# Kernel tuning notes

Hardware: AMD Instinct MI355X
Metric: run time of the kernel (lower is better)

## Reference

```python
import jax, jax.numpy as jnp
import numpy as np

N_FOOD = 50000
N_NUT = 50000
E = 800000
D = 128      # embedding_dim == hidden_dim
H = 4        # heads
C = D // H   # per-head channels
L = 2        # num_layers
NEG_SLOPE = 0.2


def _gat_conv(x_src, x_dst, ei, Wsrc, Wdst, a_src, a_dst, bias, n_dst):
    """PyG GATConv (bipartite, no self loops, concat heads, no edge_dim)."""
    hs = (x_src @ Wsrc).reshape(-1, H, C)   # [Ns, H, C]
    hd = (x_dst @ Wdst).reshape(-1, H, C)   # [Nd, H, C]
    src, dst = ei[0], ei[1]
    alpha_s = jnp.einsum('nhc,hc->nh', hs, a_src)  # [Ns, H]
    alpha_d = jnp.einsum('nhc,hc->nh', hd, a_dst)  # [Nd, H]
    e = alpha_s[src] + alpha_d[dst]                # [E, H]
    e = jax.nn.leaky_relu(e, NEG_SLOPE)
    # segment softmax over edges grouped by destination node
    emax = jax.ops.segment_max(e, dst, num_segments=n_dst)
    emax = jnp.where(jnp.isfinite(emax), emax, 0.0)
    ex = jnp.exp(e - emax[dst])
    denom = jax.ops.segment_sum(ex, dst, num_segments=n_dst)
    alpha = ex / (denom[dst] + 1e-16)              # [E, H]
    msg = hs[src] * alpha[:, :, None]              # [E, H, C]
    out = jax.ops.segment_sum(msg, dst, num_segments=n_dst)
    return out.reshape(n_dst, H * C) + bias


def setup_inputs() -> dict:
    key = jax.random.key(0)
    ks = jax.random.split(key, 16)
    w = 1.0 / np.sqrt(D)
    a = 1.0 / np.sqrt(C)
    inp = {
        'x_food': jax.random.normal(ks[0], (N_FOOD, D), jnp.float32),
        'x_nut': jax.random.normal(ks[1], (N_NUT, D), jnp.float32),
        'Wsrc_fn': jax.random.normal(ks[2], (L, D, D), jnp.float32) * w,
        'Wdst_fn': jax.random.normal(ks[3], (L, D, D), jnp.float32) * w,
        'att_src_fn': jax.random.normal(ks[4], (L, H, C), jnp.float32) * a,
        'att_dst_fn': jax.random.normal(ks[5], (L, H, C), jnp.float32) * a,
        'bias_fn': jnp.zeros((L, D), jnp.float32),
        'Wsrc_nf': jax.random.normal(ks[6], (L, D, D), jnp.float32) * w,
        'Wdst_nf': jax.random.normal(ks[7], (L, D, D), jnp.float32) * w,
        'att_src_nf': jax.random.normal(ks[8], (L, H, C), jnp.float32) * a,
        'att_dst_nf': jax.random.normal(ks[9], (L, H, C), jnp.float32) * a,
        'bias_nf': jnp.zeros((L, D), jnp.float32),
        'ei_fn': jax.random.randint(ks[10], (2, E), 0, N_FOOD, jnp.int32),  # food -> nutrient
        'ei_nf': jax.random.randint(ks[11], (2, E), 0, N_NUT, jnp.int32),   # nutrient -> food
    }
    return inp


def reference(x_food, x_nut, Wsrc_fn, Wdst_fn, att_src_fn, att_dst_fn, bias_fn,
              Wsrc_nf, Wdst_nf, att_src_nf, att_dst_nf, bias_nf, ei_fn, ei_nf):
    h_food, h_nut = x_food, x_nut
    for l in range(L):
        # relation food --contains--> nutrient (dst = nutrient)
        out_nut = _gat_conv(h_food, h_nut, ei_fn, Wsrc_fn[l], Wdst_fn[l],
                            att_src_fn[l], att_dst_fn[l], bias_fn[l], N_NUT)
        # relation nutrient --contained_in--> food (dst = food)
        out_food = _gat_conv(h_nut, h_food, ei_nf, Wsrc_nf[l], Wdst_nf[l],
                             att_src_nf[l], att_dst_nf[l], bias_nf[l], N_FOOD)
        # dropout is identity at inference; ELU activation
        h_food = jax.nn.elu(out_food)
        h_nut = jax.nn.elu(out_nut)
    return jnp.stack([h_food, h_nut])  # [2, 50000, 128]
```

## Files before the change

kernel.cpp:

```cpp
#include <hip/hip_runtime.h>
#include <math.h>

#define NNODE 50000
#define NEDGE 800000
#define DIM   128
#define NHEAD 4
#define NTILE ((NNODE + 63) / 64)
#define NBUCK 196
#define ECHUNK 196
#define CAP   6144
#define LOG2E 1.44269504088896340736f
#define NODEOCT (NNODE / 8)

typedef __bf16 bf16x8 __attribute__((ext_vector_type(8)));
typedef float  f32x4  __attribute__((ext_vector_type(4)));
typedef float  f32x2  __attribute__((ext_vector_type(2)));
typedef _Float16 f16x8 __attribute__((ext_vector_type(8)));

static __device__ __forceinline__ void bfsplit(float x, ushort& hi, ushort& lo) {
    __bf16 h = (__bf16)x;
    float hf = (float)h;
    __bf16 l = (__bf16)(x - hf);
    hi = __builtin_bit_cast(unsigned short, h);
    lo = __builtin_bit_cast(unsigned short, l);
}
static __device__ __forceinline__ ushort f2h(float x) {
    _Float16 h = (_Float16)x;
    return __builtin_bit_cast(unsigned short, h);
}
static __device__ __forceinline__ unsigned encf(float f) {
    unsigned u = __builtin_bit_cast(unsigned, f);
    return (u >> 31) ? ~u : (u | 0x80000000u);
}
static __device__ __forceinline__ float decf(unsigned x) {
    unsigned u = (x >> 31) ? (x & 0x7fffffffu) : ~x;
    return __builtin_bit_cast(float, u);
}

__global__ __launch_bounds__(256) void bhist(const int* __restrict__ eA,
                                             const int* __restrict__ eB,
                                             int* __restrict__ bcnt) {
    int rel = (int)(blockIdx.x >= ECHUNK);
    const int* dstrow = (rel ? eB : eA) + NEDGE;
    int blk = blockIdx.x - rel * ECHUNK;
    __shared__ int hist[256];
    hist[threadIdx.x] = 0;
    __syncthreads();
    int base = blk * 4096;
    #pragma unroll
    for (int k = 0; k < 16; k++) {
        int e = base + k * 256 + threadIdx.x;
        if (e < NEDGE) atomicAdd(&hist[dstrow[e] >> 8], 1);
    }
    __syncthreads();
    int h = hist[threadIdx.x];
    if (h) atomicAdd(&bcnt[rel * 256 + threadIdx.x], h);
}

__global__ __launch_bounds__(256) void bscan(const int* __restrict__ bcnt,
                                             int* __restrict__ bko, int* __restrict__ bcur,
                                             int* __restrict__ ptrA, int* __restrict__ ptrB) {
    int rel = blockIdx.x;
    __shared__ int tmp[256];
    int t = threadIdx.x;
    int v = bcnt[rel * 256 + t];
    tmp[t] = v; __syncthreads();
    for (int off = 1; off < 256; off <<= 1) {
        int a = (t >= off) ? tmp[t - off] : 0; __syncthreads();
        tmp[t] += a; __syncthreads();
    }
    int excl = tmp[t] - v;
    bko[rel * 256 + t] = excl;
    bcur[rel * 256 + t] = excl;
    if (t == 255) (rel ? ptrB : ptrA)[NNODE] = tmp[255];
}

__global__ __launch_bounds__(256) void bscatter(const int* __restrict__ eA,
                                                const int* __restrict__ eB,
                                                int* __restrict__ bcur,
                                                unsigned* __restrict__ bktA,
                                                unsigned* __restrict__ bktB) {
    int rel = (int)(blockIdx.x >= ECHUNK);
    const int* ebase = rel ? eB : eA;
    unsigned* bkt = rel ? bktB : bktA;
    int blk = blockIdx.x - rel * ECHUNK;
    __shared__ int hist[256], bas[256], cur[256];
    hist[threadIdx.x] = 0;
    __syncthreads();
    int base = blk * 4096;
    #pragma unroll
    for (int k = 0; k < 16; k++) {
        int e = base + k * 256 + threadIdx.x;
        if (e < NEDGE) atomicAdd(&hist[ebase[NEDGE + e] >> 8], 1);
    }
    __syncthreads();
    int h = hist[threadIdx.x];
    bas[threadIdx.x] = h ? atomicAdd(&bcur[rel * 256 + threadIdx.x], h) : 0;
    cur[threadIdx.x] = 0;
    __syncthreads();
    #pragma unroll
    for (int k = 0; k < 16; k++) {
        int e = base + k * 256 + threadIdx.x;
        if (e < NEDGE) {
            int s = ebase[e], d = ebase[NEDGE + e];
            int b = d >> 8;
            int loc = atomicAdd(&cur[b], 1);
            bkt[bas[b] + loc] = ((unsigned)(d & 255) << 16) | (unsigned)s;
        }
    }
}

__global__ __launch_bounds__(256) void bsort(const unsigned* __restrict__ bktA,
                                             const unsigned* __restrict__ bktB,
                                             const int* __restrict__ bko,
                                             int* __restrict__ ptrA, int* __restrict__ ptrB,
                                             ushort* __restrict__ srcA, ushort* __restrict__ srcB) {
    int rel = (int)(blockIdx.x >= NBUCK);
    const unsigned* bkt = rel ? bktB : bktA;
    int* ptr   = rel ? ptrB : ptrA;
    ushort* srcs = rel ? srcB : srcA;
    int b = blockIdx.x - rel * NBUCK;
    int beg = bko[rel * 256 + b], end = bko[rel * 256 + b + 1];
    int cnt_e = end - beg;
    __shared__ int hist[256], excl[256], cur[256];
    __shared__ unsigned sorted[CAP];
    int t = threadIdx.x;
    hist[t] = 0;
    __syncthreads();
    for (int i = t; i < cnt_e; i += 256) atomicAdd(&hist[bkt[beg + i] >> 16], 1);
    __syncthreads();
    int v = hist[t];
    excl[t] = v; __syncthreads();
    for (int off = 1; off < 256; off <<= 1) {
        int a = (t >= off) ? excl[t - off] : 0; __syncthreads();
        excl[t] += a; __syncthreads();
    }
    int ex = excl[t] - v;
    int d = b * 256 + t;
    if (d < NNODE) ptr[d] = beg + ex;
    cur[t] = ex;
    __syncthreads();
    for (int i = t; i < cnt_e; i += 256) {
        unsigned u = bkt[beg + i];
        int dl = u >> 16;
        int p = atomicAdd(&cur[dl], 1);
        if (p < CAP) sorted[p] = u;
        else srcs[beg + p] = (ushort)(u & 0xffffu);
    }
    __syncthreads();
    int lim = cnt_e < CAP ? cnt_e : CAP;
    for (int i = t; i < lim; i += 256) {
        unsigned u = sorted[i];
        srcs[beg + i] = (ushort)(u & 0xffffu);
    }
}

__global__ void prep_wav(const float* __restrict__ Wsrc_fn, const float* __restrict__ a_src_fn,
                         const float* __restrict__ Wdst_fn, const float* __restrict__ a_dst_fn,
                         const float* __restrict__ Wsrc_nf, const float* __restrict__ a_src_nf,
                         const float* __restrict__ Wdst_nf, const float* __restrict__ a_dst_nf,
                         float* __restrict__ wav) {
    int call = blockIdx.x;
    int layer = call >> 1, which = call & 1;
    const float* Ws = which ? Wsrc_nf : Wsrc_fn;
    const float* as = which ? a_src_nf : a_src_fn;
    const float* Wd = which ? Wdst_fn : Wdst_nf;
    const float* ad = which ? a_dst_fn : a_dst_nf;
    Ws += layer * DIM * DIM; Wd += layer * DIM * DIM;
    as += layer * DIM; ad += layer * DIM;
    for (int it = threadIdx.x; it < 512; it += 256) {
        int k = it >> 2, h = it & 3;
        float s = 0.f, dv = 0.f;
        #pragma unroll 8
        for (int c = 0; c < 32; c++) {
            s  += Ws[k * DIM + h * 32 + c] * as[h * 32 + c];
            dv += Wd[k * DIM + h * 32 + c] * ad[h * 32 + c];
        }
        float* o = wav + (size_t)call * DIM * 8 + k * 8;
        o[h] = s; o[h + 4] = dv;
    }
}

__global__ __launch_bounds__(256, 4) void transform_kernel(
    const float* __restrict__ XA, const float* __restrict__ WA, const float* __restrict__ wavA,
    ushort* __restrict__ HSA, float* __restrict__ ASA, float* __restrict__ ADA,
    const float* __restrict__ XB, const float* __restrict__ WB, const float* __restrict__ wavB,
    ushort* __restrict__ HSB, float* __restrict__ ASB, float* __restrict__ ADB,
    unsigned* __restrict__ Mg, int nb)
{
    int rel = (int)(blockIdx.x >= (unsigned)nb);
    const float* X  = rel ? XB : XA;
    const float* W  = rel ? WB : WA;
    const float* wav = rel ? wavB : wavA;
    ushort* HS = rel ? HSB : HSA;
    float*  AS = rel ? ASB : ASA;
    float*  AD = rel ? ADB : ADA;

    __shared__ ushort WTh[64][136], WTl[64][136];
    __shared__ ushort hsb[32][72];
    __shared__ unsigned mloc[4];

    int vb = blockIdx.x - rel * nb;
    int half = vb & 1;
    int ch = half * 64;

    for (int i = threadIdx.x; i < 64 * DIM; i += 256) {
        int col = i & 63, k = i >> 6;
        ushort hi, lo; bfsplit(W[k * DIM + ch + col], hi, lo);
        WTh[col][k] = hi; WTl[col][k] = lo;
    }
    if (threadIdx.x < 4) mloc[threadIdx.x] = 0;

    const int wv = threadIdx.x >> 6, lane = threadIdx.x & 63;
    const int lm = lane & 15, lq = lane >> 4;
    const int r0 = wv * 16;
    const int tstride = nb >> 1;

    bf16x8 wvh[4], wvl[4];
    if (half == 0) {
        #pragma unroll
        for (int kc = 0; kc < 4; kc++) {
            int k0 = kc * 32 + lq * 8;
            #pragma unroll
            for (int j = 0; j < 8; j++) {
                float w = (lm < 8) ? wav[(k0 + j) * 8 + lm] : 0.f;
                __bf16 h = (__bf16)w;
                wvh[kc][j] = h;
                wvl[kc][j] = (__bf16)(w - (float)h);
            }
        }
    }
    __syncthreads();

    auto loadX = [&](int tile, float4* dst) {
        int myrow = tile * 64 + r0 + lm;
        int rowc = myrow < NNODE ? myrow : NNODE - 1;
        const float4* Xr = (const float4*)(X + (size_t)rowc * DIM);
        #pragma unroll
        for (int kc = 0; kc < 4; kc++) {
            dst[kc * 2]     = Xr[kc * 8 + lq * 2];
            dst[kc * 2 + 1] = Xr[kc * 8 + lq * 2 + 1];
        }
    };

    auto computeTile = [&](const float4* xv, int tile) {
        int row0 = tile * 64;
        f32x4 acc[4] = {{0,0,0,0},{0,0,0,0},{0,0,0,0},{0,0,0,0}};
        f32x4 accv = {0,0,0,0};
        #pragma unroll
        for (int kc = 0; kc < 4; kc++) {
            const float* fp = (const float*)&xv[kc * 2];
            bf16x8 ah, al;
            #pragma unroll
            for (int j = 0; j < 8; j++) {
                float x = fp[j];
                __bf16 h = (__bf16)x;
                ah[j] = h;
                al[j] = (__bf16)(x - (float)h);
            }
            int k0 = kc * 32 + lq * 8;
            #pragma unroll
            for (int ct = 0; ct < 4; ct++) {
                bf16x8 bh = *(const bf16x8*)&WTh[ct * 16 + lm][k0];
                bf16x8 bl = *(const bf16x8*)&WTl[ct * 16 + lm][k0];
                acc[ct] = __builtin_amdgcn_mfma_f32_16x16x32_bf16(al, bh, acc[ct], 0, 0, 0);
                acc[ct] = __builtin_amdgcn_mfma_f32_16x16x32_bf16(ah, bl, acc[ct], 0, 0, 0);
                acc[ct] = __builtin_amdgcn_mfma_f32_16x16x32_bf16(ah, bh, acc[ct], 0, 0, 0);
            }
            if (half == 0) {
                accv = __builtin_amdgcn_mfma_f32_16x16x32_bf16(al, wvh[kc], accv, 0, 0, 0);
                accv = __builtin_amdgcn_mfma_f32_16x16x32_bf16(ah, wvl[kc], accv, 0, 0, 0);
                accv = __builtin_amdgcn_mfma_f32_16x16x32_bf16(ah, wvh[kc], accv, 0, 0, 0);
            }
        }

        if (half == 0 && lm < 8) {
            accv *= LOG2E;
            float mx4 = -INFINITY;
            #pragma unroll
            for (int r = 0; r < 4; r++) {
                int row = row0 + r0 + lq * 4 + r;
                if (row < NNODE) {
                    if (lm < 4) AS[row * 4 + lm] = accv[r];
                    else        AD[row * 4 + (lm - 4)] = accv[r];
                }
                mx4 = fmaxf(mx4, accv[r]);
            }
            if (lm < 4) atomicMax(&mloc[lm], encf(mx4));
        }

        #pragma unroll
        for (int p = 0; p < 2; p++) {
            __syncthreads();
            if ((wv >> 1) == p) {
                #pragma unroll
                for (int ct = 0; ct < 4; ct++) {
                    #pragma unroll
                    for (int r = 0; r < 4; r++)
                        hsb[(r0 & 31) + lq * 4 + r][ct * 16 + lm] = f2h(acc[ct][r]);
                }
            }
            __syncthreads();
            int lr = (int)threadIdx.x >> 3, off = ((int)threadIdx.x & 7) * 8;
            int rg = row0 + p * 32 + lr;
            if (rg < NNODE)
                *(uint4*)(HS + (size_t)rg * DIM + ch + off) = *(const uint4*)&hsb[lr][off];
        }
    };

    float4 xa[8], xb[8];
    int tile = vb >> 1;
    loadX(tile, xa);
    while (tile < NTILE) {
        if (tile + tstride < NTILE) loadX(tile + tstride, xb);
        computeTile(xa, tile);
        tile += tstride;
        if (tile >= NTILE) break;
        if (tile + tstride < NTILE) loadX(tile + tstride, xa);
        computeTile(xb, tile);
        tile += tstride;
    }

    __syncthreads();
    if (half == 0 && threadIdx.x < 4)
        atomicMax(&Mg[rel * 4 + threadIdx.x], mloc[threadIdx.x]);
}

__global__ __launch_bounds__(256) void agg_kernel(
    const ushort* __restrict__ HSA, const float* __restrict__ ASA, const float* __restrict__ ADA,
    const int* __restrict__ ptrA, const ushort* __restrict__ srcA,
    const float* __restrict__ biasA, float* __restrict__ outA,
    const ushort* __restrict__ HSB, const float* __restrict__ ASB, const float* __restrict__ ADB,
    const int* __restrict__ ptrB, const ushort* __restrict__ srcB,
    const float* __restrict__ biasB, float* __restrict__ outB,
    const unsigned* __restrict__ Mg)
{
    unsigned idx = blockIdx.x;
    int g   = (idx >> 2) & 1;
    int sub = (int)((idx >> 3) << 2) | (int)(idx & 3);
    int rel = (int)(sub >= NODEOCT);
    int bid = sub - rel * NODEOCT;

    const uint4* HS4 = (const uint4*)(rel ? HSB : HSA);
    const float* AS = rel ? ASB : ASA;
    const float* AD = rel ? ADB : ADA;
    const ushort* srcs = rel ? srcB : srcA;
    const int* ptr = rel ? ptrB : ptrA;
    const float* bias = rel ? biasB : biasA;
    float* out = rel ? outB : outA;

    int wave = threadIdx.x >> 6, lane = threadIdx.x & 63;
    int h32 = lane >> 5;
    int q  = (lane >> 3) & 3;
    int li = lane & 7;
    int hh = g * 2 + (li >> 2);
    int d = bid * 8 + wave * 2 + h32;
    int rowoff = g * 8 + li;

    float ad_h = AD[d * 4 + hh];
    float mm = decf(Mg[rel * 4 + hh]) + ad_h;
    mm = fmaxf(mm, 0.2f * mm);

    int e0 = ptr[d], e1 = ptr[d + 1];

    float acc[8] = {0.f,0.f,0.f,0.f,0.f,0.f,0.f,0.f};
    float l = 0.f;

    int e = e0;
    for (; e + 16 <= e1; e += 16) {
        int s0 = srcs[e + q],     s1 = srcs[e + 4 + q];
        int s2 = srcs[e + 8 + q], s3 = srcs[e + 12 + q];
        uint4 u0 = HS4[s0 * 16 + rowoff];
        uint4 u1 = HS4[s1 * 16 + rowoff];
        uint4 u2 = HS4[s2 * 16 + rowoff];
        uint4 u3 = HS4[s3 * 16 + rowoff];
        float a0 = AS[s0 * 4 + hh], a1 = AS[s1 * 4 + hh];
        float a2 = AS[s2 * 4 + hh], a3 = AS[s3 * 4 + hh];
        float v0 = a0 + ad_h; v0 = fmaxf(v0, 0.2f * v0);
        float v1 = a1 + ad_h; v1 = fmaxf(v1, 0.2f * v1);
        float v2 = a2 + ad_h; v2 = fmaxf(v2, 0.2f * v2);
        float v3 = a3 + ad_h; v3 = fmaxf(v3, 0.2f * v3);
        float p0 = __builtin_amdgcn_exp2f(v0 - mm);
        float p1 = __builtin_amdgcn_exp2f(v1 - mm);
        float p2 = __builtin_amdgcn_exp2f(v2 - mm);
        float p3 = __builtin_amdgcn_exp2f(v3 - mm);
        l += (p0 + p1) + (p2 + p3);
        f16x8 h0 = __builtin_bit_cast(f16x8, u0);
        f16x8 h1 = __builtin_bit_cast(f16x8, u1);
        f16x8 h2 = __builtin_bit_cast(f16x8, u2);
        f16x8 h3 = __builtin_bit_cast(f16x8, u3);
        #pragma unroll
        for (int j = 0; j < 8; j++) {
            acc[j] = __builtin_fmaf((float)h0[j], p0, acc[j]);
            acc[j] = __builtin_fmaf((float)h1[j], p1, acc[j]);
            acc[j] = __builtin_fmaf((float)h2[j], p2, acc[j]);
            acc[j] = __builtin_fmaf((float)h3[j], p3, acc[j]);
        }
    }
    for (; e + 8 <= e1; e += 8) {
        int sA = srcs[e + q], sB = srcs[e + 4 + q];
        uint4 uA = HS4[sA * 16 + rowoff];
        uint4 uB = HS4[sB * 16 + rowoff];
        float aA = AS[sA * 4 + hh], aB = AS[sB * 4 + hh];
        float vA = aA + ad_h; vA = fmaxf(vA, 0.2f * vA);
        float vB = aB + ad_h; vB = fmaxf(vB, 0.2f * vB);
        float pA = __builtin_amdgcn_exp2f(vA - mm);
        float pB = __builtin_amdgcn_exp2f(vB - mm);
        l += pA + pB;
        f16x8 hA = __builtin_bit_cast(f16x8, uA);
        f16x8 hB = __builtin_bit_cast(f16x8, uB);
        #pragma unroll
        for (int j = 0; j < 8; j++) {
            acc[j] = __builtin_fmaf((float)hA[j], pA, acc[j]);
            acc[j] = __builtin_fmaf((float)hB[j], pB, acc[j]);
        }
    }
    for (; e < e1; e += 4) {
        int ee = e + q;
        bool act = ee < e1;
        int eidx = act ? ee : e1 - 1;
        int s = srcs[eidx];
        uint4 u = HS4[s * 16 + rowoff];
        float a = AS[s * 4 + hh];
        float v = a + ad_h; v = fmaxf(v, 0.2f * v);
        float p = __builtin_amdgcn_exp2f(v - mm);
        p = act ? p : 0.f;
        l += p;
        f16x8 h = __builtin_bit_cast(f16x8, u);
        #pragma unroll
        for (int j = 0; j < 8; j++)
            acc[j] = __builtin_fmaf((float)h[j], p, acc[j]);
    }

    #pragma unroll
    for (int j = 0; j < 8; j++) {
        acc[j] += __shfl_xor(acc[j], 8, 64);
        acc[j] += __shfl_xor(acc[j], 16, 64);
    }
    l += __shfl_xor(l, 8, 64);
    l += __shfl_xor(l, 16, 64);

    if (q == 0) {
        float inv = 1.f / (l + 1e-16f);
        const float4* b4 = (const float4*)(bias + g * 64) + li * 2;
        float4 b0 = b4[0], b1 = b4[1];
        float o[8];
        o[0] = acc[0] * inv + b0.x; o[1] = acc[1] * inv + b0.y;
        o[2] = acc[2] * inv + b0.z; o[3] = acc[3] * inv + b0.w;
        o[4] = acc[4] * inv + b1.x; o[5] = acc[5] * inv + b1.y;
        o[6] = acc[6] * inv + b1.z; o[7] = acc[7] * inv + b1.w;
        #pragma unroll
        for (int j = 0; j < 8; j++)
            o[j] = o[j] > 0.f ? o[j] : __expf(o[j]) - 1.f;
        float4* o4 = (float4*)(out + (size_t)d * DIM + g * 64) + li * 2;
        o4[0] = make_float4(o[0], o[1], o[2], o[3]);
        o4[1] = make_float4(o[4], o[5], o[6], o[7]);
    }
}

extern "C" void kernel_launch(void* const* d_in, const int* in_sizes, int n_in,
                              void* d_out, int out_size, void* d_ws, size_t ws_size,
                              hipStream_t stream) {
    const float* x_food      = (const float*)d_in[0];
    const float* x_nut       = (const float*)d_in[1];
    const float* Wsrc_fn     = (const float*)d_in[2];
    const float* Wdst_fn     = (const float*)d_in[3];
    const float* att_src_fn  = (const float*)d_in[4];
    const float* att_dst_fn  = (const float*)d_in[5];
    const float* bias_fn     = (const float*)d_in[6];
    const float* Wsrc_nf     = (const float*)d_in[7];
    const float* Wdst_nf     = (const float*)d_in[8];
    const float* att_src_nf  = (const float*)d_in[9];
    const float* att_dst_nf  = (const float*)d_in[10];
    const float* bias_nf     = (const float*)d_in[11];
    const int*   ei_fn       = (const int*)d_in[12];
    const int*   ei_nf       = (const int*)d_in[13];
    float* out = (float*)d_out;

    char* ws = (char*)d_ws;
    size_t off = 0;
    auto alloc_f = [&](size_t n) { float* p = (float*)(ws + off); off += n * 4; return p; };
    auto alloc_i = [&](size_t n) { int* p = (int*)(ws + off); off += n * 4; return p; };
    auto alloc_u = [&](size_t n) { ushort* p = (ushort*)(ws + off); off += n * 2; return p; };

    float* B_food = alloc_f((size_t)NNODE * DIM);
    float* B_nut  = alloc_f((size_t)NNODE * DIM);
    ushort* HS_fn = alloc_u((size_t)NNODE * DIM);
    ushort* HS_nf = alloc_u((size_t)NNODE * DIM);
    float* AS_fn  = alloc_f(NNODE * NHEAD);
    float* AS_nf  = alloc_f(NNODE * NHEAD);
    float* AD_fn  = alloc_f(NNODE * NHEAD);
    float* AD_nf  = alloc_f(NNODE * NHEAD);
    float* wav    = alloc_f(4 * DIM * 8);
    int* ptr_fn   = alloc_i(50004);
    int* ptr_nf   = alloc_i(50004);
    ushort* srcs_fn = alloc_u(NEDGE);
    ushort* srcs_nf = alloc_u(NEDGE);
    int* bcnt     = alloc_i(512);
    unsigned* Mbuf = (unsigned*)alloc_i(16);
    int* bko      = alloc_i(512);
    int* bcur     = alloc_i(512);
    unsigned* bkt_fn = (unsigned*)B_food;
    unsigned* bkt_nf = (unsigned*)B_nut;

    hipMemsetAsync(bcnt, 0, (512 + 16) * 4, stream);
    bhist<<<2 * ECHUNK, 256, 0, stream>>>(ei_fn, ei_nf, bcnt);
    bscan<<<2, 256, 0, stream>>>(bcnt, bko, bcur, ptr_fn, ptr_nf);
    bscatter<<<2 * ECHUNK, 256, 0, stream>>>(ei_fn, ei_nf, bcur, bkt_fn, bkt_nf);
    bsort<<<2 * NBUCK, 256, 0, stream>>>(bkt_fn, bkt_nf, bko, ptr_fn, ptr_nf,
                                         srcs_fn, srcs_nf);

    prep_wav<<<4, 256, 0, stream>>>(Wsrc_fn, att_src_fn, Wdst_fn, att_dst_fn,
                                    Wsrc_nf, att_src_nf, Wdst_nf, att_dst_nf, wav);

    const int WL = DIM * DIM;
    const int TNB = 512;
    const int AGRID = 2 * 2 * NODEOCT;
    float* wav0 = wav;
    float* wav1 = wav + DIM * 8;
    float* wav2 = wav + 2 * DIM * 8;
    float* wav3 = wav + 3 * DIM * 8;

    transform_kernel<<<2 * TNB, 256, 0, stream>>>(
        x_food, Wsrc_fn, wav0, HS_fn, AS_fn, AD_nf,
        x_nut,  Wsrc_nf, wav1, HS_nf, AS_nf, AD_fn, Mbuf, TNB);
    agg_kernel<<<AGRID, 256, 0, stream>>>(
        HS_fn, AS_fn, AD_fn, ptr_fn, srcs_fn, bias_fn, B_nut,
        HS_nf, AS_nf, AD_nf, ptr_nf, srcs_nf, bias_nf, B_food, Mbuf);

    transform_kernel<<<2 * TNB, 256, 0, stream>>>(
        B_food, Wsrc_fn + WL, wav2, HS_fn, AS_fn, AD_nf,
        B_nut,  Wsrc_nf + WL, wav3, HS_nf, AS_nf, AD_fn, Mbuf + 8, TNB);
    agg_kernel<<<AGRID, 256, 0, stream>>>(
        HS_fn, AS_fn, AD_fn, ptr_fn, srcs_fn, bias_fn + DIM, out + (size_t)NNODE * DIM,
        HS_nf, AS_nf, AD_nf, ptr_nf, srcs_nf, bias_nf + DIM, out, Mbuf + 8);
}
```

Measured before the change: 396.1 us.

## Assign one wave per destination node with full-row lanes and shuffled source indices

The aggregation kernel now maps each wave to one destination node, with 16 lanes covering the full 128-channel fp16 row and 4 lane groups splitting edges. Previously each node was split across two blocks, one per pair of heads. Source indices are loaded once per 64-edge window with one coalesced load and broadcast through shuffles, replacing repeated per-lane index loads. The output is written as float2 per lane after a cross-group reduction. This removes the duplicated index and attention loads from the head split, at the cost of extra shuffles and half-length output stores.

Result: no change. 400.4 us (+1.1%).

```diff
diff --git a/kernel.cpp b/kernel.cpp
--- a/kernel.cpp
+++ b/kernel.cpp
@@ -10,11 +10,9 @@
 #define ECHUNK 196
 #define CAP   6144
 #define LOG2E 1.44269504088896340736f
-#define NODEOCT (NNODE / 8)
 
 typedef __bf16 bf16x8 __attribute__((ext_vector_type(8)));
 typedef float  f32x4  __attribute__((ext_vector_type(4)));
-typedef float  f32x2  __attribute__((ext_vector_type(2)));
 typedef _Float16 f16x8 __attribute__((ext_vector_type(8)));
 
 static __device__ __forceinline__ void bfsplit(float x, ushort& hi, ushort& lo) {
@@ -333,14 +331,9 @@
     const ushort* __restrict__ HSB, const float* __restrict__ ASB, const float* __restrict__ ADB,
     const int* __restrict__ ptrB, const ushort* __restrict__ srcB,
     const float* __restrict__ biasB, float* __restrict__ outB,
-    const unsigned* __restrict__ Mg)
+    const unsigned* __restrict__ Mg, int nb)
 {
-    unsigned idx = blockIdx.x;
-    int g   = (idx >> 2) & 1;
-    int sub = (int)((idx >> 3) << 2) | (int)(idx & 3);
-    int rel = (int)(sub >= NODEOCT);
-    int bid = sub - rel * NODEOCT;
-
+    int rel = (int)(blockIdx.x >= (unsigned)nb);
     const uint4* HS4 = (const uint4*)(rel ? HSB : HSA);
     const float* AS = rel ? ASB : ASA;
     const float* AD = rel ? ADB : ADA;
@@ -349,113 +342,101 @@
     const float* bias = rel ? biasB : biasA;
     float* out = rel ? outB : outA;
 
+    int bid = blockIdx.x - rel * nb;
     int wave = threadIdx.x >> 6, lane = threadIdx.x & 63;
-    int h32 = lane >> 5;
-    int q  = (lane >> 3) & 3;
-    int li = lane & 7;
-    int hh = g * 2 + (li >> 2);
-    int d = bid * 8 + wave * 2 + h32;
-    int rowoff = g * 8 + li;
+    int d = bid * 4 + wave;
+
+    int q  = lane >> 4;
+    int li = lane & 15;
+    int hh = li >> 2;
 
     float ad_h = AD[d * 4 + hh];
     float mm = decf(Mg[rel * 4 + hh]) + ad_h;
     mm = fmaxf(mm, 0.2f * mm);
 
     int e0 = ptr[d], e1 = ptr[d + 1];
+    int deg = e1 - e0;
 
     float acc[8] = {0.f,0.f,0.f,0.f,0.f,0.f,0.f,0.f};
     float l = 0.f;
 
-    int e = e0;
-    for (; e + 16 <= e1; e += 16) {
-        int s0 = srcs[e + q],     s1 = srcs[e + 4 + q];
-        int s2 = srcs[e + 8 + q], s3 = srcs[e + 12 + q];
-        uint4 u0 = HS4[s0 * 16 + rowoff];
-        uint4 u1 = HS4[s1 * 16 + rowoff];
-        uint4 u2 = HS4[s2 * 16 + rowoff];
-        uint4 u3 = HS4[s3 * 16 + rowoff];
-        float a0 = AS[s0 * 4 + hh], a1 = AS[s1 * 4 + hh];
-        float a2 = AS[s2 * 4 + hh], a3 = AS[s3 * 4 + hh];
-        float v0 = a0 + ad_h; v0 = fmaxf(v0, 0.2f * v0);
-        float v1 = a1 + ad_h; v1 = fmaxf(v1, 0.2f * v1);
-        float v2 = a2 + ad_h; v2 = fmaxf(v2, 0.2f * v2);
-        float v3 = a3 + ad_h; v3 = fmaxf(v3, 0.2f * v3);
-        float p0 = __builtin_amdgcn_exp2f(v0 - mm);
-        float p1 = __builtin_amdgcn_exp2f(v1 - mm);
-        float p2 = __builtin_amdgcn_exp2f(v2 - mm);
-        float p3 = __builtin_amdgcn_exp2f(v3 - mm);
-        l += (p0 + p1) + (p2 + p3);
-        f16x8 h0 = __builtin_bit_cast(f16x8, u0);
-        f16x8 h1 = __builtin_bit_cast(f16x8, u1);
-        f16x8 h2 = __builtin_bit_cast(f16x8, u2);
-        f16x8 h3 = __builtin_bit_cast(f16x8, u3);
-        #pragma unroll
-        for (int j = 0; j < 8; j++) {
-            acc[j] = __builtin_fmaf((float)h0[j], p0, acc[j]);
-            acc[j] = __builtin_fmaf((float)h1[j], p1, acc[j]);
-            acc[j] = __builtin_fmaf((float)h2[j], p2, acc[j]);
-            acc[j] = __builtin_fmaf((float)h3[j], p3, acc[j]);
-        }
-    }
-    for (; e + 8 <= e1; e += 8) {
-        int sA = srcs[e + q], sB = srcs[e + 4 + q];
-        uint4 uA = HS4[sA * 16 + rowoff];
-        uint4 uB = HS4[sB * 16 + rowoff];
-        float aA = AS[sA * 4 + hh], aB = AS[sB * 4 + hh];
-        float vA = aA + ad_h; vA = fmaxf(vA, 0.2f * vA);
-        float vB = aB + ad_h; vB = fmaxf(vB, 0.2f * vB);
-        float pA = __builtin_amdgcn_exp2f(vA - mm);
-        float pB = __builtin_amdgcn_exp2f(vB - mm);
-        l += pA + pB;
-        f16x8 hA = __builtin_bit_cast(f16x8, uA);
-        f16x8 hB = __builtin_bit_cast(f16x8, uB);
-        #pragma unroll
-        for (int j = 0; j < 8; j++) {
-            acc[j] = __builtin_fmaf((float)hA[j], pA, acc[j]);
-            acc[j] = __builtin_fmaf((float)hB[j], pB, acc[j]);
-        }
-    }
-    for (; e < e1; e += 4) {
-        int ee = e + q;
-        bool act = ee < e1;
-        int eidx = act ? ee : e1 - 1;
-        int s = srcs[eidx];
-        uint4 u = HS4[s * 16 + rowoff];
-        float a = AS[s * 4 + hh];
-        float v = a + ad_h; v = fmaxf(v, 0.2f * v);
-        float p = __builtin_amdgcn_exp2f(v - mm);
-        p = act ? p : 0.f;
-        l += p;
-        f16x8 h = __builtin_bit_cast(f16x8, u);
-        #pragma unroll
-        for (int j = 0; j < 8; j++)
-            acc[j] = __builtin_fmaf((float)h[j], p, acc[j]);
+    for (int base = 0; base < deg; base += 64) {
+        int win = deg - base; win = win < 64 ? win : 64;
+        int clamp = win - 1;
+        int sv = srcs[e0 + base + (lane < win ? lane : clamp)];
+
+        int k = 0;
+        for (; k + 16 <= win; k += 16) {
+            int i0 = k + q * 4;
+            int s0 = __shfl(sv, i0,     64);
+            int s1 = __shfl(sv, i0 + 1, 64);
+            int s2 = __shfl(sv, i0 + 2, 64);
+            int s3 = __shfl(sv, i0 + 3, 64);
+            uint4 u0 = HS4[s0 * 16 + li];
+            uint4 u1 = HS4[s1 * 16 + li];
+            uint4 u2 = HS4[s2 * 16 + li];
+            uint4 u3 = HS4[s3 * 16 + li];
+            float a0 = AS[s0 * 4 + hh], a1 = AS[s1 * 4 + hh];
+            float a2 = AS[s2 * 4 + hh], a3 = AS[s3 * 4 + hh];
+            float v0 = a0 + ad_h; v0 = fmaxf(v0, 0.2f * v0);
+            float v1 = a1 + ad_h; v1 = fmaxf(v1, 0.2f * v1);
+            float v2 = a2 + ad_h; v2 = fmaxf(v2, 0.2f * v2);
+            float v3 = a3 + ad_h; v3 = fmaxf(v3, 0.2f * v3);
+            float p0 = __builtin_amdgcn_exp2f(v0 - mm);
+            float p1 = __builtin_amdgcn_exp2f(v1 - mm);
+            float p2 = __builtin_amdgcn_exp2f(v2 - mm);
+            float p3 = __builtin_amdgcn_exp2f(v3 - mm);
+            l += (p0 + p1) + (p2 + p3);
+            f16x8 h0 = __builtin_bit_cast(f16x8, u0);
+            f16x8 h1 = __builtin_bit_cast(f16x8, u1);
+            f16x8 h2 = __builtin_bit_cast(f16x8, u2);
+            f16x8 h3 = __builtin_bit_cast(f16x8, u3);
+            #pragma unroll
+            for (int j = 0; j < 8; j++) {
+                acc[j] = __builtin_fmaf((float)h0[j], p0, acc[j]);
+                acc[j] = __builtin_fmaf((float)h1[j], p1, acc[j]);
+                acc[j] = __builtin_fmaf((float)h2[j], p2, acc[j]);
+                acc[j] = __builtin_fmaf((float)h3[j], p3, acc[j]);
+            }
+        }
+        for (; k < win; k += 4) {
+            int i = k + q;
+            bool act = i < win;
+            int s = __shfl(sv, act ? i : 0, 64);
+            uint4 u = HS4[s * 16 + li];
+            float a = AS[s * 4 + hh];
+            float v = a + ad_h; v = fmaxf(v, 0.2f * v);
+            float p = __builtin_amdgcn_exp2f(v - mm);
+            p = act ? p : 0.f;
+            l += p;
+            f16x8 h = __builtin_bit_cast(f16x8, u);
+            #pragma unroll
+            for (int j = 0; j < 8; j++)
+                acc[j] = __builtin_fmaf((float)h[j], p, acc[j]);
+        }
     }
 
     #pragma unroll
     for (int j = 0; j < 8; j++) {
-        acc[j] += __shfl_xor(acc[j], 8, 64);
         acc[j] += __shfl_xor(acc[j], 16, 64);
-    }
-    l += __shfl_xor(l, 8, 64);
+        acc[j] += __shfl_xor(acc[j], 32, 64);
+    }
     l += __shfl_xor(l, 16, 64);
-
-    if (q == 0) {
-        float inv = 1.f / (l + 1e-16f);
-        const float4* b4 = (const float4*)(bias + g * 64) + li * 2;
-        float4 b0 = b4[0], b1 = b4[1];
-        float o[8];
-        o[0] = acc[0] * inv + b0.x; o[1] = acc[1] * inv + b0.y;
-        o[2] = acc[2] * inv + b0.z; o[3] = acc[3] * inv + b0.w;
-        o[4] = acc[4] * inv + b1.x; o[5] = acc[5] * inv + b1.y;
-        o[6] = acc[6] * inv + b1.z; o[7] = acc[7] * inv + b1.w;
-        #pragma unroll
-        for (int j = 0; j < 8; j++)
-            o[j] = o[j] > 0.f ? o[j] : __expf(o[j]) - 1.f;
-        float4* o4 = (float4*)(out + (size_t)d * DIM + g * 64) + li * 2;
-        o4[0] = make_float4(o[0], o[1], o[2], o[3]);
-        o4[1] = make_float4(o[4], o[5], o[6], o[7]);
-    }
+    l += __shfl_xor(l, 32, 64);
+
+    float a0, a1;
+    if      (q == 0) { a0 = acc[0]; a1 = acc[1]; }
+    else if (q == 1) { a0 = acc[2]; a1 = acc[3]; }
+    else if (q == 2) { a0 = acc[4]; a1 = acc[5]; }
+    else             { a0 = acc[6]; a1 = acc[7]; }
+    float inv = 1.f / (l + 1e-16f);
+    int c0 = li * 8 + q * 2;
+    float2 b2 = *(const float2*)&bias[c0];
+    float o0 = a0 * inv + b2.x;
+    float o1 = a1 * inv + b2.y;
+    o0 = o0 > 0.f ? o0 : __expf(o0) - 1.f;
+    o1 = o1 > 0.f ? o1 : __expf(o1) - 1.f;
+    *(float2*)&out[(size_t)d * DIM + c0] = make_float2(o0, o1);
 }
 
 extern "C" void kernel_launch(void* const* d_in, const int* in_sizes, int n_in,
@@ -515,7 +496,7 @@
 
     const int WL = DIM * DIM;
     const int TNB = 512;
-    const int AGRID = 2 * 2 * NODEOCT;
+    const int ANB = NNODE / 4;
     float* wav0 = wav;
     float* wav1 = wav + DIM * 8;
     float* wav2 = wav + 2 * DIM * 8;
@@ -524,14 +505,14 @@
     transform_kernel<<<2 * TNB, 256, 0, stream>>>(
         x_food, Wsrc_fn, wav0, HS_fn, AS_fn, AD_nf,
         x_nut,  Wsrc_nf, wav1, HS_nf, AS_nf, AD_fn, Mbuf, TNB);
-    agg_kernel<<<AGRID, 256, 0, stream>>>(
+    agg_kernel<<<2 * ANB, 256, 0, stream>>>(
         HS_fn, AS_fn, AD_fn, ptr_fn, srcs_fn, bias_fn, B_nut,
-        HS_nf, AS_nf, AD_nf, ptr_nf, srcs_nf, bias_nf, B_food, Mbuf);
+        HS_nf, AS_nf, AD_nf, ptr_nf, srcs_nf, bias_nf, B_food, Mbuf, ANB);
 
     transform_kernel<<<2 * TNB, 256, 0, stream>>>(
         B_food, Wsrc_fn + WL, wav2, HS_fn, AS_fn, AD_nf,
         B_nut,  Wsrc_nf + WL, wav3, HS_nf, AS_nf, AD_fn, Mbuf + 8, TNB);
-    agg_kernel<<<AGRID, 256, 0, stream>>>(
+    agg_kernel<<<2 * ANB, 256, 0, stream>>>(
         HS_fn, AS_fn, AD_fn, ptr_fn, srcs_fn, bias_fn + DIM, out + (size_t)NNODE * DIM,
-        HS_nf, AS_nf, AD_nf, ptr_nf, srcs_nf, bias_nf + DIM, out, Mbuf + 8);
-}
+        HS_nf, AS_nf, AD_nf, ptr_nf, srcs_nf, bias_nf + DIM, out, Mbuf + 8, ANB);
+}
```
